# Performance work log

Hardware: AMD Instinct MI355X
Metric: run time of the kernel (lower is better)

Reference implementation:

```python
import jax, jax.numpy as jnp
import numpy as np

N_NODES = 100000


def gcn_conv(x, W, b, src, dst, n_nodes):
    # PyG GCNConv: x' = x @ W; symmetric deg^-1/2 normalization with self-loops; scatter-add; + bias
    h = x @ W  # [N, out]
    ones = jnp.ones(dst.shape[0], dtype=h.dtype)
    deg = jax.ops.segment_sum(ones, dst, num_segments=n_nodes)  # in-degree incl. self-loops
    dinv = jnp.where(deg > 0, jax.lax.rsqrt(deg), 0.0)
    norm = dinv[src] * dinv[dst]                      # [E]
    msgs = h[src] * norm[:, None]                     # gather + scale, [E, out]
    out = jax.ops.segment_sum(msgs, dst, num_segments=n_nodes)  # scatter-add
    return out + b


def setup_inputs() -> dict:
    key = jax.random.key(0)
    ks = jax.random.split(key, 8)
    n, e, din, dh, dout = N_NODES, 1600000, 32, 64, 5
    x = jax.random.normal(ks[0], (n, din), dtype=jnp.float32)
    edge_index = jax.random.randint(ks[1], (2, e), 0, n, dtype=jnp.int64)
    W1 = jax.random.normal(ks[2], (din, dh), dtype=jnp.float32) * (1.0 / np.sqrt(din))
    b1 = jax.random.normal(ks[3], (dh,), dtype=jnp.float32) * 0.02
    W2 = jax.random.normal(ks[4], (dh, dh), dtype=jnp.float32) * (1.0 / np.sqrt(dh))
    b2 = jax.random.normal(ks[5], (dh,), dtype=jnp.float32) * 0.02
    Wfc = jax.random.normal(ks[6], (dh, dout), dtype=jnp.float32) * (1.0 / np.sqrt(dh))
    bfc = jax.random.normal(ks[7], (dout,), dtype=jnp.float32) * 0.02
    return {"x": x, "edge_index": edge_index, "W1": W1, "b1": b1,
            "W2": W2, "b2": b2, "Wfc": Wfc, "bfc": bfc}


def reference(x, edge_index, W1, b1, W2, b2, Wfc, bfc):
    n = x.shape[0]
    loops = jnp.arange(n, dtype=edge_index.dtype)
    src = jnp.concatenate([edge_index[0], loops])  # add self-loops (PyG default)
    dst = jnp.concatenate([edge_index[1], loops])
    h = jax.nn.relu(gcn_conv(x, W1, b1, src, dst, n))
    h = jax.nn.relu(gcn_conv(h, W2, b2, src, dst, n))
    g = jnp.mean(h, axis=0)          # mean pool over nodes, [hidden]
    logits = g @ Wfc + bfc           # [output_dim]
    return jax.nn.log_softmax(logits, axis=0)
```

## Files before the change

kernel.cpp:

```cpp
#include <hip/hip_runtime.h>
#include <math.h>

#define NBLK 256

typedef unsigned int uint;
typedef __attribute__((ext_vector_type(8))) short short8;
typedef __attribute__((ext_vector_type(4))) float f32x4;
typedef __attribute__((ext_vector_type(2))) float f32x2;

#if defined(__has_builtin)
#if __has_builtin(__builtin_amdgcn_cvt_pk_f32_fp8) && __has_builtin(__builtin_amdgcn_cvt_pk_fp8_f32)
#define HW_FP8 1
#endif
#endif
#ifndef HW_FP8
#define HW_FP8 0
#endif

__device__ __forceinline__ uint pack_bf16(float a, float b) {
    uint ua = __float_as_uint(a), ub = __float_as_uint(b);
    ua = (ua + 0x7fffu + ((ua >> 16) & 1u)) >> 16;
    ub = (ub + 0x7fffu + ((ub >> 16) & 1u)) >> 16;
    return ua | (ub << 16);
}

__device__ __forceinline__ uint fp8_enc_sw(float v) {
    uint u = __float_as_uint(v);
    uint s = (u >> 24) & 0x80u;
    uint a = u & 0x7fffffffu;
    if (a < 0x3BF80000u) return s;
    if (a >= 0x43F80000u) return s | 0x7Fu;
    uint r = a + 0x0007FFFFu + ((a >> 20) & 1u);
    uint e8 = (r >> 23) - 120u;
    return s | (e8 << 3) | ((r >> 20) & 7u);
}
__device__ __forceinline__ float fp8_dec_sw(uint b) {
    uint t = b & 0x7fu;
    uint h = ((b & 0x80u) << 8) | (t ? ((t << 7) + 0x2000u) : 0u);
    return (float)__builtin_bit_cast(_Float16, (unsigned short)h);
}

__device__ __forceinline__ uint fp8x2_enc(float a, float b) {
#if HW_FP8
    return (uint)__builtin_amdgcn_cvt_pk_fp8_f32(a, b, 0, false);
#else
    return fp8_enc_sw(a) | (fp8_enc_sw(b) << 8);
#endif
}

#if HW_FP8
#define DEC8ACC(U)                                                         \
    do {                                                                   \
        f32x2 p0 = __builtin_amdgcn_cvt_pk_f32_fp8((int)(U).x, 0);         \
        f32x2 p1 = __builtin_amdgcn_cvt_pk_f32_fp8((int)(U).x, 1);         \
        f32x2 p2 = __builtin_amdgcn_cvt_pk_f32_fp8((int)(U).y, 0);         \
        f32x2 p3 = __builtin_amdgcn_cvt_pk_f32_fp8((int)(U).y, 1);         \
        a0 += p0.x; a1 += p0.y; a2 += p1.x; a3 += p1.y;                    \
        a4 += p2.x; a5 += p2.y; a6 += p3.x; a7 += p3.y;                    \
    } while (0)
#else
#define DEC8ACC(U)                                                         \
    do {                                                                   \
        a0 += fp8_dec_sw((U).x); a1 += fp8_dec_sw((U).x >> 8);             \
        a2 += fp8_dec_sw((U).x >> 16); a3 += fp8_dec_sw((U).x >> 24);      \
        a4 += fp8_dec_sw((U).y); a5 += fp8_dec_sw((U).y >> 8);             \
        a6 += fp8_dec_sw((U).y >> 16); a7 += fp8_dec_sw((U).y >> 24);      \
    } while (0)
#endif


__global__ void pass_hist(const int* __restrict__ dst, int* __restrict__ cnt,
                          int E, int nbucket, int chunk) {
    extern __shared__ int h[];
    int blk = blockIdx.x;
    for (int i = threadIdx.x; i < nbucket; i += blockDim.x) h[i] = 0;
    __syncthreads();
    int lo = blk * chunk, hi = min(lo + chunk, E);
    for (int e = lo + threadIdx.x; e < hi; e += blockDim.x)
        atomicAdd(&h[dst[e] >> 8], 1);
    __syncthreads();
    for (int i = threadIdx.x; i < nbucket; i += blockDim.x)
        cnt[i * NBLK + blk] = h[i];
}

__global__ void row_scan(int* __restrict__ cnt, int* __restrict__ totals) {
    __shared__ int lds[NBLK];
    int b = blockIdx.x, t = threadIdx.x;
    int v = cnt[b * NBLK + t];
    lds[t] = v;
    __syncthreads();
    for (int off = 1; off < NBLK; off <<= 1) {
        int y = (t >= off) ? lds[t - off] : 0;
        __syncthreads();
        lds[t] += y;
        __syncthreads();
    }
    cnt[b * NBLK + t] = lds[t] - v;
    if (t == NBLK - 1) totals[b] = lds[NBLK - 1];
}

__global__ void total_scan(int* __restrict__ totals, int nb) {
    __shared__ int lds[256];
    __shared__ int carry;
    int t = threadIdx.x;
    if (t == 0) carry = 0;
    __syncthreads();
    for (int c = 0; c < nb; c += 256) {
        int v = (c + t < nb) ? totals[c + t] : 0;
        lds[t] = v;
        __syncthreads();
        for (int off = 1; off < 256; off <<= 1) {
            int y = (t >= off) ? lds[t - off] : 0;
            __syncthreads();
            lds[t] += y;
            __syncthreads();
        }
        if (c + t < nb) totals[c + t] = carry + lds[t] - v;
        __syncthreads();
        if (t == 0) carry += lds[255];
        __syncthreads();
    }
    if (t == 0) totals[nb] = carry;
}

__global__ void pass_scatter(const int* __restrict__ src, const int* __restrict__ dst,
                             const int* __restrict__ cnt, const int* __restrict__ totals,
                             int* __restrict__ bucketed, int E, int nbucket, int chunk) {
    extern __shared__ int lcur[];
    int blk = blockIdx.x;
    for (int i = threadIdx.x; i < nbucket; i += blockDim.x)
        lcur[i] = cnt[i * NBLK + blk] + totals[i];
    __syncthreads();
    int lo = blk * chunk, hi = min(lo + chunk, E);
    for (int e = lo + threadIdx.x; e < hi; e += blockDim.x) {
        int s = src[e], d = dst[e];
        int pos = atomicAdd(&lcur[d >> 8], 1);
        bucketed[pos] = (s << 8) | (d & 255);
    }
}

__global__ void bucket_finalize(const int* __restrict__ bucketed, const int* __restrict__ totals,
                                int* __restrict__ rowptr, float* __restrict__ dinv,
                                int* __restrict__ csr_src, const float* __restrict__ x,
                                uint* __restrict__ xfp8, int n) {
    __shared__ int deg[256], sc[256], lcur[256];
    int b = blockIdx.x, t = threadIdx.x;
    int base = totals[b], bend = totals[b + 1];
    deg[t] = 0;
    __syncthreads();
    for (int i = base + t; i < bend; i += 256)
        atomicAdd(&deg[bucketed[i] & 255], 1);
    __syncthreads();
    int v = deg[t];
    sc[t] = v;
    __syncthreads();
    for (int off = 1; off < 256; off <<= 1) {
        int y = (t >= off) ? sc[t - off] : 0;
        __syncthreads();
        sc[t] += y;
        __syncthreads();
    }
    int ex = sc[t] - v;
    lcur[t] = ex;
    int node = b * 256 + t;
    if (node < n) {
        float dfac = rsqrtf((float)(v + 1));
        rowptr[node] = base + ex;
        dinv[node] = dfac;
        const float4* xr = reinterpret_cast<const float4*>(x + (size_t)node * 32);
        uint* xo = xfp8 + (size_t)node * 8;
#pragma unroll
        for (int w = 0; w < 8; ++w) {
            float4 xv = xr[w];
            uint lo = fp8x2_enc(xv.x * dfac, xv.y * dfac);
            uint hi = fp8x2_enc(xv.z * dfac, xv.w * dfac);
            xo[w] = (lo & 0xffffu) | (hi << 16);
        }
    }
    if (b == 0 && t == 0) rowptr[n] = totals[gridDim.x];
    __syncthreads();
    for (int i = base + t; i < bend; i += 256) {
        int p = bucketed[i];
        int pos = atomicAdd(&lcur[p & 255], 1);
        csr_src[base + pos] = p >> 8;
    }
}


__device__ __forceinline__ short8 make_bfrag(const float* __restrict__ W, int kbase, int col) {
    uint w0 = pack_bf16(W[(kbase + 0) * 64 + col], W[(kbase + 1) * 64 + col]);
    uint w1 = pack_bf16(W[(kbase + 2) * 64 + col], W[(kbase + 3) * 64 + col]);
    uint w2 = pack_bf16(W[(kbase + 4) * 64 + col], W[(kbase + 5) * 64 + col]);
    uint w3 = pack_bf16(W[(kbase + 6) * 64 + col], W[(kbase + 7) * 64 + col]);
    uint4 u; u.x = w0; u.y = w1; u.z = w2; u.w = w3;
    return __builtin_bit_cast(short8, u);
}

__global__ __launch_bounds__(256, 4) void agg1_gemm1_fused(
    const int* __restrict__ rowptr, const int* __restrict__ csr_src,
    const float* __restrict__ dinv, const uint* __restrict__ xfp8,
    const float* __restrict__ W, const float* __restrict__ bias,
    uint* __restrict__ outw, int n, int npad) {
    __shared__ uint lds[64 * 16];
    int t = threadIdx.x;
    {
        int v4 = t >> 2, q = t & 3;
        int node = blockIdx.x * 64 + v4;
        const uint* fs = xfp8 + q * 2;
        float a0 = 0.f, a1 = 0.f, a2 = 0.f, a3 = 0.f,
              a4 = 0.f, a5 = 0.f, a6 = 0.f, a7 = 0.f;
        float di = 0.f;
        int k = 0, end = 0;
        if (node < n) {
            k = rowptr[node]; end = rowptr[node + 1];
            di = dinv[node];
            uint2 w = *reinterpret_cast<const uint2*>(fs + (size_t)node * 8);
            DEC8ACC(w);
        }
        for (; k + 4 <= end; k += 4) {
            int s0 = csr_src[k], s1 = csr_src[k + 1], s2 = csr_src[k + 2], s3 = csr_src[k + 3];
            uint2 u0 = *reinterpret_cast<const uint2*>(fs + (size_t)s0 * 8);
            uint2 u1 = *reinterpret_cast<const uint2*>(fs + (size_t)s1 * 8);
            uint2 u2 = *reinterpret_cast<const uint2*>(fs + (size_t)s2 * 8);
            uint2 u3 = *reinterpret_cast<const uint2*>(fs + (size_t)s3 * 8);
            DEC8ACC(u0); DEC8ACC(u1); DEC8ACC(u2); DEC8ACC(u3);
        }
        for (; k < end; ++k) {
            int s = csr_src[k];
            uint2 u = *reinterpret_cast<const uint2*>(fs + (size_t)s * 8);
            DEC8ACC(u);
        }
        uint4 o;
        o.x = pack_bf16(a0 * di, a1 * di);
        o.y = pack_bf16(a2 * di, a3 * di);
        o.z = pack_bf16(a4 * di, a5 * di);
        o.w = pack_bf16(a6 * di, a7 * di);
        *reinterpret_cast<uint4*>(&lds[v4 * 16 + q * 4]) = o;
    }
    __syncthreads();
    int lane = t & 63, wv = t >> 6;
    int rowbase = blockIdx.x * 64 + wv * 16;
    int r16 = lane & 15, g4 = lane >> 4;
    short8 a = __builtin_bit_cast(short8,
        *reinterpret_cast<const uint4*>(&lds[(wv * 16 + r16) * 16 + g4 * 4]));
    int kbase = g4 * 8;
    float dr[4];
#pragma unroll
    for (int r = 0; r < 4; ++r) {
        int row = rowbase + g4 * 4 + r;
        dr[r] = (row < n) ? dinv[row] : 0.f;
    }
#pragma unroll
    for (int nt = 0; nt < 4; ++nt) {
        int col = nt * 16 + r16;
        short8 b = make_bfrag(W, kbase, col);
        f32x4 z = {0.f, 0.f, 0.f, 0.f};
        f32x4 acc = __builtin_amdgcn_mfma_f32_16x16x32_bf16(a, b, z, 0, 0, 0);
        float bcol = bias[col];
#pragma unroll
        for (int r = 0; r < 4; ++r) {
            int row = rowbase + g4 * 4 + r;
            float v = fmaxf(acc[r] + bcol, 0.f) * dr[r];
            float vn = __shfl_xor(v, 1);
            uint e = fp8x2_enc(v, vn) & 0xffffu;
            uint e2 = __shfl_xor(e, 2);
            if ((r16 & 3) == 0)
                outw[(size_t)row * 16 + (col >> 2)] = e | (e2 << 16);
        }
    }
}

__global__ __launch_bounds__(512, 2) void agg2_gather64(
    const int* __restrict__ rowptr, const int* __restrict__ csr_src,
    const float* __restrict__ dinv, const uint* __restrict__ feat,
    uint* __restrict__ out, int n, int npad) {
    int node = blockIdx.x * 64 + (threadIdx.x >> 3);
    if (node >= n) return;
    int q = threadIdx.x & 7;
    const uint* fs = feat + q * 2;
    int k = rowptr[node], end = rowptr[node + 1];
    float a0 = 0.f, a1 = 0.f, a2 = 0.f, a3 = 0.f, a4 = 0.f, a5 = 0.f, a6 = 0.f, a7 = 0.f;
    {
        uint2 w = *reinterpret_cast<const uint2*>(fs + (size_t)node * 16);
        DEC8ACC(w);
    }
    for (; k + 4 <= end; k += 4) {
        int s0 = csr_src[k], s1 = csr_src[k + 1], s2 = csr_src[k + 2], s3 = csr_src[k + 3];
        uint2 u0 = *reinterpret_cast<const uint2*>(fs + (size_t)s0 * 16);
        uint2 u1 = *reinterpret_cast<const uint2*>(fs + (size_t)s1 * 16);
        uint2 u2 = *reinterpret_cast<const uint2*>(fs + (size_t)s2 * 16);
        uint2 u3 = *reinterpret_cast<const uint2*>(fs + (size_t)s3 * 16);
        DEC8ACC(u0); DEC8ACC(u1); DEC8ACC(u2); DEC8ACC(u3);
    }
    for (; k < end; ++k) {
        int s = csr_src[k];
        uint2 u = *reinterpret_cast<const uint2*>(fs + (size_t)s * 16);
        DEC8ACC(u);
    }
    float di = dinv[node];
    uint4 o;
    o.x = pack_bf16(a0 * di, a1 * di);
    o.y = pack_bf16(a2 * di, a3 * di);
    o.z = pack_bf16(a4 * di, a5 * di);
    o.w = pack_bf16(a6 * di, a7 * di);
    *reinterpret_cast<uint4*>(
        out + ((size_t)(q >> 1) * npad + node) * 8 + (q & 1) * 4) = o;
}

__global__ __launch_bounds__(256) void gemm2_mfma_pool(const uint* __restrict__ A,
                                                       const float* __restrict__ W,
                                                       const float* __restrict__ bias,
                                                       float* __restrict__ pool_part,
                                                       int n, int npad) {
    __shared__ float sblk[64];
    int t = threadIdx.x;
    if (t < 64) sblk[t] = 0.f;
    __syncthreads();
    int lane = t & 63, wv = t >> 6;
    int rowbase = blockIdx.x * 64 + wv * 16;
    int r16 = lane & 15, g4 = lane >> 4;
    size_t roff = (size_t)(rowbase + r16) * 8 + (g4 & 1) * 4;
    size_t sstride = (size_t)npad * 8;
    short8 a0 = __builtin_bit_cast(short8,
        *reinterpret_cast<const uint4*>(A + (size_t)(g4 >> 1) * sstride + roff));
    short8 a1 = __builtin_bit_cast(short8,
        *reinterpret_cast<const uint4*>(A + (size_t)(2 + (g4 >> 1)) * sstride + roff));
#pragma unroll
    for (int nt = 0; nt < 4; ++nt) {
        int col = nt * 16 + r16;
        short8 b0 = make_bfrag(W, g4 * 8, col);
        short8 b1 = make_bfrag(W, 32 + g4 * 8, col);
        f32x4 z = {0.f, 0.f, 0.f, 0.f};
        f32x4 acc = __builtin_amdgcn_mfma_f32_16x16x32_bf16(a0, b0, z, 0, 0, 0);
        acc = __builtin_amdgcn_mfma_f32_16x16x32_bf16(a1, b1, acc, 0, 0, 0);
        float bcol = bias[col];
        float part = 0.f;
#pragma unroll
        for (int r = 0; r < 4; ++r) {
            int row = rowbase + g4 * 4 + r;
            float v = fmaxf(acc[r] + bcol, 0.f);
            part += (row < n) ? v : 0.f;
        }
        atomicAdd(&sblk[col], part);
    }
    __syncthreads();
    if (t < 64) pool_part[(size_t)blockIdx.x * 64 + t] = sblk[t];
}

__global__ __launch_bounds__(256) void pool_reduce(const float* __restrict__ pool_part,
                                                   int nblk, float* __restrict__ part2) {
    __shared__ float sd[256];
    int t = threadIdx.x;
    int col = t & 63, grp = t >> 6;
    int row0 = blockIdx.x * 4 + grp;
    float acc = 0.f;
    for (int b = row0; b < nblk; b += 256) acc += pool_part[(size_t)b * 64 + col];
    sd[t] = acc;
    __syncthreads();
    if (t < 64)
        part2[(size_t)blockIdx.x * 64 + t] = sd[t] + sd[t + 64] + sd[t + 128] + sd[t + 192];
}

__global__ __launch_bounds__(512) void final_head(const float* __restrict__ part2,
                                                  const float* __restrict__ Wfc,
                                                  const float* __restrict__ bfc,
                                                  float* __restrict__ out, int n) {
    __shared__ float red[512];
    __shared__ float gsh[64];
    __shared__ float logits[5];
    int t = threadIdx.x;
    int col = t & 63, grp = t >> 6;
    float acc = 0.f;
#pragma unroll
    for (int i = 0; i < 8; ++i) acc += part2[(size_t)(grp * 8 + i) * 64 + col];
    red[t] = acc;
    __syncthreads();
    if (t < 64) {
        float s = 0.f;
#pragma unroll
        for (int gI = 0; gI < 8; ++gI) s += red[gI * 64 + t];
        gsh[t] = s;
    }
    __syncthreads();
    if (t < 5) {
        float a = bfc[t];
        float invn = 1.0f / (float)n;
        for (int k = 0; k < 64; ++k) a += (gsh[k] * invn) * Wfc[k * 5 + t];
        logits[t] = a;
    }
    __syncthreads();
    if (t == 0) {
        float m = logits[0];
        for (int i = 1; i < 5; ++i) m = fmaxf(m, logits[i]);
        float s = 0.0f;
        for (int i = 0; i < 5; ++i) s += expf(logits[i] - m);
        float lse = m + logf(s);
        for (int i = 0; i < 5; ++i) out[i] = logits[i] - lse;
    }
}


extern "C" void kernel_launch(void* const* d_in, const int* in_sizes, int n_in,
                              void* d_out, int out_size, void* d_ws, size_t ws_size,
                              hipStream_t stream) {
    const float* x   = (const float*)d_in[0];
    const int*   ei  = (const int*)d_in[1];
    const float* W1  = (const float*)d_in[2];
    const float* b1  = (const float*)d_in[3];
    const float* W2  = (const float*)d_in[4];
    const float* b2  = (const float*)d_in[5];
    const float* Wfc = (const float*)d_in[6];
    const float* bfc = (const float*)d_in[7];
    float* out = (float*)d_out;

    const int n = in_sizes[0] / 32;
    const int E = in_sizes[1] / 2;
    const int* src = ei;
    const int* dst = ei + E;
    const int npad = (n + 63) & ~63;
    const int nbucket = (n + 255) >> 8;
    const int chunk = (E + NBLK - 1) / NBLK;
    const int nchunk = (n + 63) / 64;

    int*   csr_src = (int*)d_ws;
    int*   rowptr  = csr_src + E;
    float* dinv    = (float*)(rowptr + n + 1);
    int*   cnt     = (int*)(dinv + n);
    int*   totals  = cnt + (size_t)nbucket * NBLK;
    size_t offw    = (size_t)(totals + nbucket + 1 - (int*)d_ws);
    offw           = (offw + 15) & ~(size_t)15;
    uint*  xfp8    = (uint*)d_ws + offw;
    uint*  h1fp8   = xfp8 + (size_t)npad * 8;
    uint*  agg2    = h1fp8 + (size_t)npad * 16;
    float* pool_part = (float*)(agg2 + (size_t)4 * npad * 8);
    float* part2   = pool_part + (size_t)nchunk * 64;
    int*   bucketed = (int*)agg2;

    const int B = 256;
    const size_t lds_b = (size_t)nbucket * sizeof(int);

    pass_hist<<<NBLK, B, lds_b, stream>>>(dst, cnt, E, nbucket, chunk);
    row_scan<<<nbucket, NBLK, 0, stream>>>(cnt, totals);
    total_scan<<<1, B, 0, stream>>>(totals, nbucket);
    pass_scatter<<<NBLK, B, lds_b, stream>>>(src, dst, cnt, totals, bucketed, E, nbucket, chunk);
    bucket_finalize<<<nbucket, B, 0, stream>>>(bucketed, totals, rowptr, dinv, csr_src,
                                               x, xfp8, n);

    agg1_gemm1_fused<<<nchunk, B, 0, stream>>>(rowptr, csr_src, dinv, xfp8, W1, b1,
                                               h1fp8, n, npad);

    agg2_gather64<<<nchunk, 512, 0, stream>>>(rowptr, csr_src, dinv, h1fp8, agg2, n, npad);
    gemm2_mfma_pool<<<nchunk, B, 0, stream>>>(agg2, W2, b2, pool_part, n, npad);

    pool_reduce<<<64, B, 0, stream>>>(pool_part, nchunk, part2);
    final_head<<<1, 512, 0, stream>>>(part2, Wfc, bfc, out, n);
}
```

Baseline: 115.3 us.

## Stage bucket scatter in LDS and fuse pool reduction via atomics

pass_scatter now builds a local histogram per block, sorts its edge chunk by bucket into LDS, then writes each bucket's run to global memory contiguously. The aim is to coalesce the scattered bucketed stores. The separate pool_reduce kernel is removed: gemm2 atomically accumulates block partials into 64 rows of part2, which total_scan zeroes beforehand. This adds a serial prefix loop in one thread and a binary search per element, and makes the float summation order nondeterministic.

Measured after the change: 206.1 us. 78.8% more time.

```diff
diff --git a/kernel.cpp b/kernel.cpp
--- a/kernel.cpp
+++ b/kernel.cpp
@@ -99,10 +99,11 @@
     if (t == NBLK - 1) totals[b] = lds[NBLK - 1];
 }
 
-__global__ void total_scan(int* __restrict__ totals, int nb) {
+__global__ void total_scan(int* __restrict__ totals, int nb, float* __restrict__ part2) {
     __shared__ int lds[256];
     __shared__ int carry;
     int t = threadIdx.x;
+    for (int i = t; i < 64 * 64; i += 256) part2[i] = 0.f;
     if (t == 0) carry = 0;
     __syncthreads();
     for (int c = 0; c < nb; c += 256) {
@@ -123,19 +124,47 @@
     if (t == 0) totals[nb] = carry;
 }
 
-__global__ void pass_scatter(const int* __restrict__ src, const int* __restrict__ dst,
-                             const int* __restrict__ cnt, const int* __restrict__ totals,
-                             int* __restrict__ bucketed, int E, int nbucket, int chunk) {
-    extern __shared__ int lcur[];
-    int blk = blockIdx.x;
-    for (int i = threadIdx.x; i < nbucket; i += blockDim.x)
-        lcur[i] = cnt[i * NBLK + blk] + totals[i];
-    __syncthreads();
+__global__ __launch_bounds__(256) void pass_scatter(
+    const int* __restrict__ src, const int* __restrict__ dst,
+    const int* __restrict__ cnt, const int* __restrict__ totals,
+    int* __restrict__ bucketed, int E, int nbucket, int chunk) {
+    __shared__ int lbase[512];
+    __shared__ int lcur[512];
+    __shared__ int gofs[512];
+    extern __shared__ int edges[];
+    int blk = blockIdx.x, t = threadIdx.x;
     int lo = blk * chunk, hi = min(lo + chunk, E);
-    for (int e = lo + threadIdx.x; e < hi; e += blockDim.x) {
+    int m = hi - lo;
+    for (int i = t; i < nbucket; i += 256) lbase[i] = 0;
+    __syncthreads();
+    for (int e = lo + t; e < hi; e += 256)
+        atomicAdd(&lbase[dst[e] >> 8], 1);
+    __syncthreads();
+    if (t == 0) {
+        int run = 0;
+        for (int b = 0; b < nbucket; ++b) {
+            int c = lbase[b];
+            lbase[b] = run;
+            gofs[b] = totals[b] + cnt[b * NBLK + blk] - run;
+            run += c;
+        }
+    }
+    __syncthreads();
+    for (int i = t; i < nbucket; i += 256) lcur[i] = lbase[i];
+    __syncthreads();
+    for (int e = lo + t; e < hi; e += 256) {
         int s = src[e], d = dst[e];
         int pos = atomicAdd(&lcur[d >> 8], 1);
-        bucketed[pos] = (s << 8) | (d & 255);
+        edges[pos] = (s << 8) | (d & 255);
+    }
+    __syncthreads();
+    for (int i = t; i < m; i += 256) {
+        int loB = 0, hiB = nbucket;
+        while (hiB - loB > 1) {
+            int mid = (loB + hiB) >> 1;
+            if (lbase[mid] <= i) loB = mid; else hiB = mid;
+        }
+        bucketed[gofs[loB] + i] = edges[i];
     }
 }
 
@@ -310,7 +339,7 @@
 __global__ __launch_bounds__(256) void gemm2_mfma_pool(const uint* __restrict__ A,
                                                        const float* __restrict__ W,
                                                        const float* __restrict__ bias,
-                                                       float* __restrict__ pool_part,
+                                                       float* __restrict__ part2,
                                                        int n, int npad) {
     __shared__ float sblk[64];
     int t = threadIdx.x;
@@ -344,21 +373,7 @@
         atomicAdd(&sblk[col], part);
     }
     __syncthreads();
-    if (t < 64) pool_part[(size_t)blockIdx.x * 64 + t] = sblk[t];
-}
-
-__global__ __launch_bounds__(256) void pool_reduce(const float* __restrict__ pool_part,
-                                                   int nblk, float* __restrict__ part2) {
-    __shared__ float sd[256];
-    int t = threadIdx.x;
-    int col = t & 63, grp = t >> 6;
-    int row0 = blockIdx.x * 4 + grp;
-    float acc = 0.f;
-    for (int b = row0; b < nblk; b += 256) acc += pool_part[(size_t)b * 64 + col];
-    sd[t] = acc;
-    __syncthreads();
-    if (t < 64)
-        part2[(size_t)blockIdx.x * 64 + t] = sd[t] + sd[t + 64] + sd[t + 128] + sd[t + 192];
+    if (t < 64) atomicAdd(&part2[(size_t)(blockIdx.x & 63) * 64 + t], sblk[t]);
 }
 
 __global__ __launch_bounds__(512) void final_head(const float* __restrict__ part2,
@@ -432,17 +447,18 @@
     uint*  xfp8    = (uint*)d_ws + offw;
     uint*  h1fp8   = xfp8 + (size_t)npad * 8;
     uint*  agg2    = h1fp8 + (size_t)npad * 16;
-    float* pool_part = (float*)(agg2 + (size_t)4 * npad * 8);
-    float* part2   = pool_part + (size_t)nchunk * 64;
+    float* part2   = (float*)(agg2 + (size_t)4 * npad * 8);
     int*   bucketed = (int*)agg2;
 
     const int B = 256;
     const size_t lds_b = (size_t)nbucket * sizeof(int);
+    const size_t lds_edges = (size_t)chunk * sizeof(int);
 
     pass_hist<<<NBLK, B, lds_b, stream>>>(dst, cnt, E, nbucket, chunk);
     row_scan<<<nbucket, NBLK, 0, stream>>>(cnt, totals);
-    total_scan<<<1, B, 0, stream>>>(totals, nbucket);
-    pass_scatter<<<NBLK, B, lds_b, stream>>>(src, dst, cnt, totals, bucketed, E, nbucket, chunk);
+    total_scan<<<1, B, 0, stream>>>(totals, nbucket, part2);
+    pass_scatter<<<NBLK, B, lds_edges, stream>>>(src, dst, cnt, totals, bucketed,
+                                                 E, nbucket, chunk);
     bucket_finalize<<<nbucket, B, 0, stream>>>(bucketed, totals, rowptr, dinv, csr_src,
                                                x, xfp8, n);
 
@@ -450,8 +466,7 @@
                                                h1fp8, n, npad);
 
     agg2_gather64<<<nchunk, 512, 0, stream>>>(rowptr, csr_src, dinv, h1fp8, agg2, n, npad);
-    gemm2_mfma_pool<<<nchunk, B, 0, stream>>>(agg2, W2, b2, pool_part, n, npad);
-
-    pool_reduce<<<64, B, 0, stream>>>(pool_part, nchunk, part2);
+    gemm2_mfma_pool<<<nchunk, B, 0, stream>>>(agg2, W2, b2, part2, n, npad);
+
     final_head<<<1, 512, 0, stream>>>(part2, Wfc, bfc, out, n);
 }
```
